# Kernel optimization log

Measured on AMD Instinct MI355X. Metric: run time of the kernel, lower is better.

The kernel has to match this reference:

```python
import jax, jax.numpy as jnp
import numpy as np

B, S, DIM = 2, 2048, 2048
N_HEADS, N_KV = 32, 8
HEAD_DIM = DIM // N_HEADS
N_GROUPS = N_HEADS // N_KV

def setup_inputs() -> dict:
    key = jax.random.key(0)
    kx, kq, kk, kv, ko = jax.random.split(key, 5)
    scale = 1.0 / np.sqrt(DIM)
    return {
        "x": jax.random.normal(kx, (B, S, DIM), dtype=jnp.float32),
        "Wq": jax.random.normal(kq, (DIM, DIM), dtype=jnp.float32) * scale,
        "Wk": jax.random.normal(kk, (DIM, N_KV * HEAD_DIM), dtype=jnp.float32) * scale,
        "Wv": jax.random.normal(kv, (DIM, N_KV * HEAD_DIM), dtype=jnp.float32) * scale,
        "Wo": jax.random.normal(ko, (DIM, DIM), dtype=jnp.float32) * scale,
    }

def reference(x, Wq, Wk, Wv, Wo):
    b, s, _ = x.shape
    sm_scale = HEAD_DIM ** -0.5
    # projections; q grouped as [B, Hk, G, S, D] so kv head i serves q heads i*G..i*G+G-1
    # (matches torch repeat_interleave(n_groups, dim=1))
    q = (x @ Wq).reshape(b, s, N_KV, N_GROUPS, HEAD_DIM)
    k = (x @ Wk).reshape(b, s, N_KV, HEAD_DIM)
    v = (x @ Wv).reshape(b, s, N_KV, HEAD_DIM)
    scores = jnp.einsum("bqhgd,bkhd->bhgqk", q, k) * sm_scale  # [B,Hk,G,S,S]
    attn = jax.nn.softmax(scores, axis=-1)
    out = jnp.einsum("bhgqk,bkhd->bqhgd", attn, v)  # [B,S,Hk,G,D]
    out = out.reshape(b, s, DIM)
    return out @ Wo
```

## Files before the change

kernel.cpp:

```cpp
#include <hip/hip_runtime.h>
#include <hip/hip_bf16.h>

typedef __bf16 bf16x8 __attribute__((ext_vector_type(8)));
typedef float floatx4 __attribute__((ext_vector_type(4)));

#define DIM   2048
#define SEQ   2048
#define BATCH 2
#define NKV   8
#define NGRP  4
#define HDIM  64
#define KVDIM (NKV * HDIM)
#define QKVD  3072

__device__ __forceinline__ ushort f2bf(float f) {
  union { float f; unsigned u; } x; x.f = f;
  return (ushort)((x.u + 0x7fffu + ((x.u >> 16) & 1u)) >> 16);
}
__device__ __forceinline__ unsigned pack_bf2(float a, float b) {
  union { float f; unsigned u; } x, y; x.f = a; y.f = b;
  unsigned ua = x.u + 0x8000u, ub = y.u + 0x8000u;
  return __builtin_amdgcn_perm(ub, ua, 0x07060302);
}
__device__ __forceinline__ unsigned pack_bf2_rn(float a, float b) {
  __hip_bfloat162 h = __float22bfloat162_rn(make_float2(a, b));
  union { __hip_bfloat162 h; unsigned u; } cv; cv.h = h; return cv.u;
}

typedef const __attribute__((address_space(1))) void* gas_t;
typedef __attribute__((address_space(3))) void* las_t;
__device__ __forceinline__ void gload_lds16(const ushort* g, ushort* l) {
  __builtin_amdgcn_global_load_lds((gas_t)g, (las_t)l, 16, 0, 0);
}

__global__ __launch_bounds__(256) void cvt_f2b(
    const float* __restrict__ in, ushort* __restrict__ out)
{
  int i = blockIdx.x * 256 + threadIdx.x;
  const float4* p = (const float4*)in + (size_t)i * 2;
  float4 f0 = p[0], f1 = p[1];
  uint4 v;
  v.x = pack_bf2(f0.x, f0.y); v.y = pack_bf2(f0.z, f0.w);
  v.z = pack_bf2(f1.x, f1.y); v.w = pack_bf2(f1.z, f1.w);
  ((uint4*)out)[i] = v;
}

__global__ __launch_bounds__(256) void transpose_f2b(
    const float* __restrict__ in, ushort* __restrict__ out, int R, int C)
{
  __shared__ ushort tileT[64][72];
  int tr = blockIdx.y * 64;
  int tc = blockIdx.x * 64;
  int row = threadIdx.x >> 2;
  int c16 = (threadIdx.x & 3) * 16;

  ushort arr[16];
  const float* src = in + (size_t)(tr + row) * C + tc + c16;
#pragma unroll
  for (int q = 0; q < 4; ++q) {
    float4 f = *(const float4*)(src + q * 4);
    arr[q * 4 + 0] = f2bf(f.x); arr[q * 4 + 1] = f2bf(f.y);
    arr[q * 4 + 2] = f2bf(f.z); arr[q * 4 + 3] = f2bf(f.w);
  }
  int rot = row & 15;
#pragma unroll
  for (int j = 0; j < 16; ++j) {
    int i2 = (j + rot) & 15;
    tileT[c16 + i2][row] = arr[i2];
  }
  __syncthreads();
  ushort* dst = out + (size_t)(tc + row) * R + tr + c16;
  *(uint4*)dst       = *(const uint4*)&tileT[row][c16];
  *(uint4*)(dst + 8) = *(const uint4*)&tileT[row][c16 + 8];
}

__global__ __launch_bounds__(256) void transpose_b2b(
    const ushort* __restrict__ in, ushort* __restrict__ out,
    int R, int C, int in_stride, size_t in_batch, size_t out_batch)
{
  __shared__ ushort tileT[64][72];
  in  += (size_t)blockIdx.z * in_batch;
  out += (size_t)blockIdx.z * out_batch;
  int tr = blockIdx.y * 64;
  int tc = blockIdx.x * 64;
  int row = threadIdx.x >> 2;
  int c16 = (threadIdx.x & 3) * 16;

  ushort arr[16];
  const ushort* src = in + (size_t)(tr + row) * in_stride + tc + c16;
  *(uint4*)&arr[0] = *(const uint4*)src;
  *(uint4*)&arr[8] = *(const uint4*)(src + 8);
  int rot = row & 15;
#pragma unroll
  for (int j = 0; j < 16; ++j) {
    int i2 = (j + rot) & 15;
    tileT[c16 + i2][row] = arr[i2];
  }
  __syncthreads();
  ushort* dst = out + (size_t)(tc + row) * R + tr + c16;
  *(uint4*)dst       = *(const uint4*)&tileT[row][c16];
  *(uint4*)(dst + 8) = *(const uint4*)&tileT[row][c16 + 8];
}

template<bool CF32>
__global__ __launch_bounds__(256) void gemm_lds(
    const ushort* __restrict__ A, const ushort* __restrict__ Bt,
    void* __restrict__ Cv, int M, int N, int K)
{
  __shared__ ushort As[128 * 32];
  __shared__ ushort Bs[128 * 32];
  int tid  = threadIdx.x;
  int bm   = blockIdx.y * 128;
  int bn   = blockIdx.x * 128;
  int wv   = tid >> 6;
  int ln   = tid & 63;
  int wr   = (wv >> 1) * 64;
  int wc   = (wv & 1) * 64;
  int l15  = ln & 15;
  int quad = ln >> 4;

  int r4 = ln >> 2;
  int c8 = (ln & 3) * 8;
  const ushort* Ag0 = A  + (size_t)(bm + 32 * wv +      r4) * K + c8;
  const ushort* Ag1 = A  + (size_t)(bm + 32 * wv + 16 + r4) * K + c8;
  const ushort* Bg0 = Bt + (size_t)(bn + 32 * wv +      r4) * K + c8;
  const ushort* Bg1 = Bt + (size_t)(bn + 32 * wv + 16 + r4) * K + c8;
  ushort* Al0 = As + 1024 * wv +       ln * 8;
  ushort* Al1 = As + 1024 * wv + 512 + ln * 8;
  ushort* Bl0 = Bs + 1024 * wv +       ln * 8;
  ushort* Bl1 = Bs + 1024 * wv + 512 + ln * 8;

  floatx4 acc[4][4];
#pragma unroll
  for (int i = 0; i < 4; ++i)
#pragma unroll
    for (int j = 0; j < 4; ++j) acc[i][j] = floatx4{0,0,0,0};

  for (int k0 = 0; k0 < K; k0 += 32) {
    __syncthreads();
    gload_lds16(Ag0, Al0);
    gload_lds16(Ag1, Al1);
    gload_lds16(Bg0, Bl0);
    gload_lds16(Bg1, Bl1);
    Ag0 += 32; Ag1 += 32; Bg0 += 32; Bg1 += 32;
    __syncthreads();

    bf16x8 a[4], b[4];
#pragma unroll
    for (int t = 0; t < 4; ++t) {
      a[t] = *(const bf16x8*)&As[(wr + t * 16 + l15) * 32 + quad * 8];
      b[t] = *(const bf16x8*)&Bs[(wc + t * 16 + l15) * 32 + quad * 8];
    }
#pragma unroll
    for (int mt = 0; mt < 4; ++mt)
#pragma unroll
      for (int nt = 0; nt < 4; ++nt)
        acc[mt][nt] = __builtin_amdgcn_mfma_f32_16x16x32_bf16(a[mt], b[nt], acc[mt][nt], 0, 0, 0);
  }

#pragma unroll
  for (int mt = 0; mt < 4; ++mt)
#pragma unroll
    for (int nt = 0; nt < 4; ++nt)
#pragma unroll
      for (int r = 0; r < 4; ++r) {
        size_t idx = (size_t)(bm + wr + mt * 16 + quad * 4 + r) * N
                     + bn + wc + nt * 16 + l15;
        if (CF32) ((float*)Cv)[idx] = acc[mt][nt][r];
        else      ((ushort*)Cv)[idx] = f2bf(acc[mt][nt][r]);
      }
}

#define BM 64
#define BN 64
#define BK 32
#define KP 40

template<bool AF32, bool CF32>
__global__ __launch_bounds__(256) void gemm_abt(
    const void* __restrict__ Av, const ushort* __restrict__ Bt,
    void* __restrict__ Cv, int M, int N, int K)
{
  __shared__ ushort As[BM * KP];
  __shared__ ushort Bs[BN * KP];
  int tid  = threadIdx.x;
  int bm   = blockIdx.y * BM;
  int bn   = blockIdx.x * BN;
  int wave = tid >> 6;
  int lane = tid & 63;
  int wr   = (wave >> 1) * 32;
  int wc   = (wave & 1) * 32;
  int l15  = lane & 15;
  int k8   = (lane >> 4) * 8;

  int srow = tid >> 2;
  int scol = (tid & 3) * 8;

  const float*  Af = (const float*)Av  + (size_t)(bm + srow) * K + scol;
  const ushort* Ah = (const ushort*)Av + (size_t)(bm + srow) * K + scol;
  const ushort* Bp = Bt + (size_t)(bn + srow) * K + scol;

  floatx4 acc00 = {0,0,0,0}, acc01 = {0,0,0,0}, acc10 = {0,0,0,0}, acc11 = {0,0,0,0};

  uint4 av, bv;
  if (AF32) {
    float4 f0 = *(const float4*)Af;
    float4 f1 = *(const float4*)(Af + 4);
    av.x = pack_bf2(f0.x, f0.y); av.y = pack_bf2(f0.z, f0.w);
    av.z = pack_bf2(f1.x, f1.y); av.w = pack_bf2(f1.z, f1.w);
  } else {
    av = *(const uint4*)Ah;
  }
  bv = *(const uint4*)Bp;

  for (int k0 = 0; k0 < K; k0 += BK) {
    __syncthreads();
    *(uint4*)&As[srow * KP + scol] = av;
    *(uint4*)&Bs[srow * KP + scol] = bv;
    __syncthreads();
    if (k0 + BK < K) {
      Af += BK; Ah += BK; Bp += BK;
      if (AF32) {
        float4 f0 = *(const float4*)Af;
        float4 f1 = *(const float4*)(Af + 4);
        av.x = pack_bf2(f0.x, f0.y); av.y = pack_bf2(f0.z, f0.w);
        av.z = pack_bf2(f1.x, f1.y); av.w = pack_bf2(f1.z, f1.w);
      } else {
        av = *(const uint4*)Ah;
      }
      bv = *(const uint4*)Bp;
    }
    bf16x8 a0 = *(const bf16x8*)&As[(wr +      l15) * KP + k8];
    bf16x8 a1 = *(const bf16x8*)&As[(wr + 16 + l15) * KP + k8];
    bf16x8 b0 = *(const bf16x8*)&Bs[(wc +      l15) * KP + k8];
    bf16x8 b1 = *(const bf16x8*)&Bs[(wc + 16 + l15) * KP + k8];
    acc00 = __builtin_amdgcn_mfma_f32_16x16x32_bf16(a0, b0, acc00, 0, 0, 0);
    acc01 = __builtin_amdgcn_mfma_f32_16x16x32_bf16(a0, b1, acc01, 0, 0, 0);
    acc10 = __builtin_amdgcn_mfma_f32_16x16x32_bf16(a1, b0, acc10, 0, 0, 0);
    acc11 = __builtin_amdgcn_mfma_f32_16x16x32_bf16(a1, b1, acc11, 0, 0, 0);
  }

  int rbase = (lane >> 4) * 4;
#pragma unroll
  for (int r = 0; r < 4; ++r) {
    size_t row0 = (size_t)(bm + wr +      rbase + r) * N + bn + wc;
    size_t row1 = (size_t)(bm + wr + 16 + rbase + r) * N + bn + wc;
    if (CF32) {
      float* C = (float*)Cv;
      C[row0 +      l15] = acc00[r];
      C[row0 + 16 + l15] = acc01[r];
      C[row1 +      l15] = acc10[r];
      C[row1 + 16 + l15] = acc11[r];
    } else {
      ushort* C = (ushort*)Cv;
      C[row0 +      l15] = f2bf(acc00[r]);
      C[row0 + 16 + l15] = f2bf(acc01[r]);
      C[row1 +      l15] = f2bf(acc10[r]);
      C[row1 + 16 + l15] = f2bf(acc11[r]);
    }
  }
}

#define GKP 40
template<bool AF32, bool CF32>
__global__ __launch_bounds__(256) void gemm128(
    const void* __restrict__ Av, const ushort* __restrict__ Bt,
    void* __restrict__ Cv, int M, int N, int K)
{
  __shared__ ushort As[128 * GKP];
  __shared__ ushort Bs[128 * GKP];
  int tid  = threadIdx.x;
  int bm   = blockIdx.y * 128;
  int bn   = blockIdx.x * 128;
  int wave = tid >> 6;
  int lane = tid & 63;
  int wr   = (wave >> 1) * 64;
  int wc   = (wave & 1) * 64;
  int l15  = lane & 15;
  int quad = lane >> 4;
  int k8   = quad * 8;

  int srow = tid >> 1;
  int scol = (tid & 1) * 16;

  const float*  Af = (const float*)Av  + (size_t)(bm + srow) * K + scol;
  const ushort* Ah = (const ushort*)Av + (size_t)(bm + srow) * K + scol;
  const ushort* Bp = Bt + (size_t)(bn + srow) * K + scol;

  floatx4 acc[4][4];
#pragma unroll
  for (int i = 0; i < 4; ++i)
#pragma unroll
    for (int j = 0; j < 4; ++j) acc[i][j] = floatx4{0,0,0,0};

  uint4 av0, av1, bv0, bv1;
  if (AF32) {
    float4 f0 = *(const float4*)Af,      f1 = *(const float4*)(Af + 4);
    float4 f2 = *(const float4*)(Af + 8), f3 = *(const float4*)(Af + 12);
    av0.x = pack_bf2(f0.x, f0.y); av0.y = pack_bf2(f0.z, f0.w);
    av0.z = pack_bf2(f1.x, f1.y); av0.w = pack_bf2(f1.z, f1.w);
    av1.x = pack_bf2(f2.x, f2.y); av1.y = pack_bf2(f2.z, f2.w);
    av1.z = pack_bf2(f3.x, f3.y); av1.w = pack_bf2(f3.z, f3.w);
  } else {
    av0 = *(const uint4*)Ah; av1 = *(const uint4*)(Ah + 8);
  }
  bv0 = *(const uint4*)Bp; bv1 = *(const uint4*)(Bp + 8);

  for (int k0 = 0; k0 < K; k0 += 32) {
    __syncthreads();
    *(uint4*)&As[srow * GKP + scol]     = av0;
    *(uint4*)&As[srow * GKP + scol + 8] = av1;
    *(uint4*)&Bs[srow * GKP + scol]     = bv0;
    *(uint4*)&Bs[srow * GKP + scol + 8] = bv1;
    __syncthreads();
    if (k0 + 32 < K) {
      Af += 32; Ah += 32; Bp += 32;
      if (AF32) {
        float4 f0 = *(const float4*)Af,      f1 = *(const float4*)(Af + 4);
        float4 f2 = *(const float4*)(Af + 8), f3 = *(const float4*)(Af + 12);
        av0.x = pack_bf2(f0.x, f0.y); av0.y = pack_bf2(f0.z, f0.w);
        av0.z = pack_bf2(f1.x, f1.y); av0.w = pack_bf2(f1.z, f1.w);
        av1.x = pack_bf2(f2.x, f2.y); av1.y = pack_bf2(f2.z, f2.w);
        av1.z = pack_bf2(f3.x, f3.y); av1.w = pack_bf2(f3.z, f3.w);
      } else {
        av0 = *(const uint4*)Ah; av1 = *(const uint4*)(Ah + 8);
      }
      bv0 = *(const uint4*)Bp; bv1 = *(const uint4*)(Bp + 8);
    }
    bf16x8 a[4], b[4];
#pragma unroll
    for (int t = 0; t < 4; ++t) {
      a[t] = *(const bf16x8*)&As[(wr + t * 16 + l15) * GKP + k8];
      b[t] = *(const bf16x8*)&Bs[(wc + t * 16 + l15) * GKP + k8];
    }
#pragma unroll
    for (int mt = 0; mt < 4; ++mt)
#pragma unroll
      for (int nt = 0; nt < 4; ++nt)
        acc[mt][nt] = __builtin_amdgcn_mfma_f32_16x16x32_bf16(a[mt], b[nt], acc[mt][nt], 0, 0, 0);
  }

#pragma unroll
  for (int mt = 0; mt < 4; ++mt)
#pragma unroll
    for (int nt = 0; nt < 4; ++nt)
#pragma unroll
      for (int r = 0; r < 4; ++r) {
        size_t idx = (size_t)(bm + wr + mt * 16 + quad * 4 + r) * N
                     + bn + wc + nt * 16 + l15;
        if (CF32) ((float*)Cv)[idx] = acc[mt][nt][r];
        else      ((ushort*)Cv)[idx] = f2bf(acc[mt][nt][r]);
      }
}

#define QP 72
#define PP 72

__global__ __launch_bounds__(256) void gqa_attn(
    const ushort* __restrict__ q_buf,
    const ushort* __restrict__ k_buf,
    const ushort* __restrict__ vT,
    ushort* __restrict__ attn)
{
  __shared__ __align__(16) ushort Qs[64 * QP];
  __shared__ __align__(16) ushort Ks[64 * QP];
  __shared__ __align__(16) ushort Vs[64 * QP];
  __shared__ __align__(16) ushort Ps[4][16 * PP];

  int bid = blockIdx.x;
  int qt  = bid & 31;
  int g   = (bid >> 5) & 3;
  int h   = (bid >> 7) & 7;
  int b   = bid >> 10;

  int tid  = threadIdx.x;
  int wave = tid >> 6;
  int lane = tid & 63;
  int l15  = lane & 15;
  int quad = lane >> 4;
  int k8   = quad * 8;

  int srow = tid >> 2;
  int c16  = (tid & 3) * 16;

  {
    const ushort* src = q_buf + (size_t)(b * SEQ + qt * 64 + srow) * DIM
                        + (h * NGRP + g) * HDIM + c16;
    *(uint4*)&Qs[srow * QP + c16]     = *(const uint4*)src;
    *(uint4*)&Qs[srow * QP + c16 + 8] = *(const uint4*)(src + 8);
  }
  __syncthreads();

  bf16x8 bq0 = *(const bf16x8*)&Qs[(wave * 16 + l15) * QP + k8];
  bf16x8 bq1 = *(const bf16x8*)&Qs[(wave * 16 + l15) * QP + 32 + k8];

  float lpart = 0.f;
  floatx4 oarr[4] = {{0,0,0,0},{0,0,0,0},{0,0,0,0},{0,0,0,0}};

  const ushort* kp = k_buf + (size_t)(b * SEQ + srow) * KVDIM + h * HDIM + c16;
  const ushort* vp = vT + ((size_t)(b * NKV + h) * HDIM + srow) * SEQ + c16;

  uint4 kv0 = *(const uint4*)kp;
  uint4 kv1 = *(const uint4*)(kp + 8);
  uint4 vv0 = *(const uint4*)vp;
  uint4 vv1 = *(const uint4*)(vp + 8);

  ushort* Pw = &Ps[wave][0];

  for (int kt = 0; kt < SEQ / 64; ++kt) {
    __syncthreads();
    *(uint4*)&Ks[srow * QP + c16]     = kv0;
    *(uint4*)&Ks[srow * QP + c16 + 8] = kv1;
    *(uint4*)&Vs[srow * QP + c16]     = vv0;
    *(uint4*)&Vs[srow * QP + c16 + 8] = vv1;
    __syncthreads();
    if (kt + 1 < SEQ / 64) {
      kp += (size_t)64 * KVDIM;
      vp += 64;
      kv0 = *(const uint4*)kp;
      kv1 = *(const uint4*)(kp + 8);
      vv0 = *(const uint4*)vp;
      vv1 = *(const uint4*)(vp + 8);
    }

    floatx4 sarr[4];
#pragma unroll
    for (int nt = 0; nt < 4; ++nt) {
      bf16x8 ak0 = *(const bf16x8*)&Ks[(nt * 16 + l15) * QP + k8];
      bf16x8 ak1 = *(const bf16x8*)&Ks[(nt * 16 + l15) * QP + 32 + k8];
      floatx4 s = {0.f, 0.f, 0.f, 0.f};
      s = __builtin_amdgcn_mfma_f32_16x16x32_bf16(ak0, bq0, s, 0, 0, 0);
      s = __builtin_amdgcn_mfma_f32_16x16x32_bf16(ak1, bq1, s, 0, 0, 0);
      sarr[nt] = s;
    }

#pragma unroll
    for (int nt = 0; nt < 4; ++nt) {
      float p0 = __expf(sarr[nt][0] * 0.125f);
      float p1 = __expf(sarr[nt][1] * 0.125f);
      float p2 = __expf(sarr[nt][2] * 0.125f);
      float p3 = __expf(sarr[nt][3] * 0.125f);
      lpart += (p0 + p1) + (p2 + p3);
      uint2 pw;
      pw.x = pack_bf2(p0, p1);
      pw.y = pack_bf2(p2, p3);
      *(uint2*)&Pw[l15 * PP + nt * 16 + quad * 4] = pw;
    }

    bf16x8 ap0 = *(const bf16x8*)&Pw[l15 * PP + k8];
    bf16x8 ap1 = *(const bf16x8*)&Pw[l15 * PP + 32 + k8];
#pragma unroll
    for (int dt = 0; dt < 4; ++dt) {
      bf16x8 bv0q = *(const bf16x8*)&Vs[(dt * 16 + l15) * QP + k8];
      bf16x8 bv1q = *(const bf16x8*)&Vs[(dt * 16 + l15) * QP + 32 + k8];
      oarr[dt] = __builtin_amdgcn_mfma_f32_16x16x32_bf16(ap0, bv0q, oarr[dt], 0, 0, 0);
      oarr[dt] = __builtin_amdgcn_mfma_f32_16x16x32_bf16(ap1, bv1q, oarr[dt], 0, 0, 0);
    }
  }

  float ls = lpart;
  ls += __shfl_xor(ls, 16, 64);
  ls += __shfl_xor(ls, 32, 64);

  __syncthreads();
  float* Lw = (float*)Pw;
  if (quad == 0) Lw[l15] = ls;
  __syncthreads();

#pragma unroll
  for (int r = 0; r < 4; ++r) {
    float inv = 1.0f / Lw[quad * 4 + r];
    int q = qt * 64 + wave * 16 + quad * 4 + r;
    size_t rowoff = (size_t)(b * SEQ + q) * DIM + (h * NGRP + g) * HDIM;
#pragma unroll
    for (int dt = 0; dt < 4; ++dt)
      attn[rowoff + dt * 16 + l15] = f2bf(oarr[dt][r] * inv);
  }
}

__global__ __launch_bounds__(256, 2) void gqa_attn3(
    const ushort* __restrict__ qkv,
    const ushort* __restrict__ vT,
    ushort* __restrict__ attn)
{
  __shared__ __align__(16) ushort Ks[64 * QP];
  __shared__ __align__(16) ushort Vs[64 * QP];
  __shared__ __align__(16) ushort Ps[4][16 * PP];

  int bid = blockIdx.x;
  int qt  = bid & 31;
  int h   = (bid >> 5) & 7;
  int b   = bid >> 8;

  int tid  = threadIdx.x;
  int wave = tid >> 6;
  int lane = tid & 63;
  int l15  = lane & 15;
  int quad = lane >> 4;
  int k8   = quad * 8;

  int srow = tid >> 2;
  int c16  = (tid & 3) * 16;

  bf16x8 bq[NGRP][2];
  {
    const ushort* qrow = qkv + (size_t)(b * SEQ + qt * 64 + wave * 16 + l15) * QKVD
                         + h * NGRP * HDIM;
#pragma unroll
    for (int g = 0; g < NGRP; ++g) {
      bq[g][0] = *(const bf16x8*)(qrow + g * HDIM + k8);
      bq[g][1] = *(const bf16x8*)(qrow + g * HDIM + 32 + k8);
    }
  }
#pragma unroll
  for (int g = 0; g < NGRP; ++g)
#pragma unroll
    for (int j = 0; j < 2; ++j)
#pragma unroll
      for (int e = 0; e < 8; ++e)
        bq[g][j][e] = (__bf16)((float)bq[g][j][e] * 0.125f);

  bf16x8 vones;
#pragma unroll
  for (int i = 0; i < 8; ++i) vones[i] = (__bf16)1.0f;

  floatx4 lacc[NGRP];
  floatx4 oacc[NGRP][4];
#pragma unroll
  for (int g = 0; g < NGRP; ++g) {
    lacc[g] = floatx4{0,0,0,0};
#pragma unroll
    for (int dt = 0; dt < 4; ++dt) oacc[g][dt] = floatx4{0,0,0,0};
  }

  const ushort* kp = qkv + (size_t)(b * SEQ + srow) * QKVD + DIM + h * HDIM + c16;
  const ushort* vp = vT + ((size_t)(b * NKV + h) * HDIM + srow) * SEQ + c16;

  uint4 kv0 = *(const uint4*)kp;
  uint4 kv1 = *(const uint4*)(kp + 8);
  uint4 vv0 = *(const uint4*)vp;
  uint4 vv1 = *(const uint4*)(vp + 8);

  ushort* Pw = &Ps[wave][0];

  for (int kt = 0; kt < SEQ / 64; ++kt) {
    __syncthreads();
    *(uint4*)&Ks[srow * QP + c16]     = kv0;
    *(uint4*)&Ks[srow * QP + c16 + 8] = kv1;
    *(uint4*)&Vs[srow * QP + c16]     = vv0;
    *(uint4*)&Vs[srow * QP + c16 + 8] = vv1;
    __syncthreads();
    if (kt + 1 < SEQ / 64) {
      kp += (size_t)64 * QKVD;
      vp += 64;
      kv0 = *(const uint4*)kp;
      kv1 = *(const uint4*)(kp + 8);
      vv0 = *(const uint4*)vp;
      vv1 = *(const uint4*)(vp + 8);
    }

    bf16x8 ak[4][2], av[4][2];
#pragma unroll
    for (int t = 0; t < 4; ++t) {
      ak[t][0] = *(const bf16x8*)&Ks[(t * 16 + l15) * QP + k8];
      ak[t][1] = *(const bf16x8*)&Ks[(t * 16 + l15) * QP + 32 + k8];
      av[t][0] = *(const bf16x8*)&Vs[(t * 16 + l15) * QP + k8];
      av[t][1] = *(const bf16x8*)&Vs[(t * 16 + l15) * QP + 32 + k8];
    }

#pragma unroll
    for (int g = 0; g < NGRP; ++g) {
#pragma unroll
      for (int nt = 0; nt < 4; ++nt) {
        floatx4 s = {0.f, 0.f, 0.f, 0.f};
        s = __builtin_amdgcn_mfma_f32_16x16x32_bf16(ak[nt][0], bq[g][0], s, 0, 0, 0);
        s = __builtin_amdgcn_mfma_f32_16x16x32_bf16(ak[nt][1], bq[g][1], s, 0, 0, 0);
        float p0 = __expf(s[0]);
        float p1 = __expf(s[1]);
        float p2 = __expf(s[2]);
        float p3 = __expf(s[3]);
        uint2 pw;
        pw.x = pack_bf2_rn(p0, p1);
        pw.y = pack_bf2_rn(p2, p3);
        *(uint2*)&Pw[l15 * PP + nt * 16 + quad * 4] = pw;
      }

      asm volatile("" ::: "memory");

      bf16x8 ap0 = *(const bf16x8*)&Pw[l15 * PP + k8];
      bf16x8 ap1 = *(const bf16x8*)&Pw[l15 * PP + 32 + k8];
      lacc[g] = __builtin_amdgcn_mfma_f32_16x16x32_bf16(ap0, vones, lacc[g], 0, 0, 0);
      lacc[g] = __builtin_amdgcn_mfma_f32_16x16x32_bf16(ap1, vones, lacc[g], 0, 0, 0);
#pragma unroll
      for (int dt = 0; dt < 4; ++dt) {
        oacc[g][dt] = __builtin_amdgcn_mfma_f32_16x16x32_bf16(ap0, av[dt][0], oacc[g][dt], 0, 0, 0);
        oacc[g][dt] = __builtin_amdgcn_mfma_f32_16x16x32_bf16(ap1, av[dt][1], oacc[g][dt], 0, 0, 0);
      }

      asm volatile("" ::: "memory");
    }
  }

#pragma unroll
  for (int g = 0; g < NGRP; ++g) {
#pragma unroll
    for (int r = 0; r < 4; ++r) {
      float inv = 1.0f / lacc[g][r];
      int q = qt * 64 + wave * 16 + quad * 4 + r;
      size_t rowoff = (size_t)(b * SEQ + q) * DIM + (h * NGRP + g) * HDIM;
#pragma unroll
      for (int dt = 0; dt < 4; ++dt)
        attn[rowoff + dt * 16 + l15] = f2bf(oacc[g][dt][r] * inv);
    }
  }
}

extern "C" void kernel_launch(void* const* d_in, const int* in_sizes, int n_in,
                              void* d_out, int out_size, void* d_ws, size_t ws_size,
                              hipStream_t stream)
{
  (void)in_sizes; (void)n_in; (void)out_size;
  const float* x  = (const float*)d_in[0];
  const float* Wq = (const float*)d_in[1];
  const float* Wk = (const float*)d_in[2];
  const float* Wv = (const float*)d_in[3];
  const float* Wo = (const float*)d_in[4];
  float*  outf = (float*)d_out;
  ushort* ob   = (ushort*)d_out;
  ushort* ws16 = (ushort*)d_ws;

  const size_t Mi = 1024 * 1024;
  dim3 blk(256);
  const int M = BATCH * SEQ;

  if (ws_size >= 40u * Mi) {
    ushort* WqkvT = ws16;
    ushort* WoT   = ws16 + 8 * Mi;
    ushort* xb    = ws16 + 12 * Mi;
    ushort* ao    = ws16 + 12 * Mi;
    ushort* qkv   = ob;
    ushort* vt    = ob + 12 * Mi;

    cvt_f2b<<<dim3((M * DIM) / (8 * 256)), blk, 0, stream>>>(x, xb);
    transpose_f2b<<<dim3(DIM / 64,   DIM / 64), blk, 0, stream>>>(Wq, WqkvT, DIM, DIM);
    transpose_f2b<<<dim3(KVDIM / 64, DIM / 64), blk, 0, stream>>>(Wk, WqkvT + 4 * Mi, DIM, KVDIM);
    transpose_f2b<<<dim3(KVDIM / 64, DIM / 64), blk, 0, stream>>>(Wv, WqkvT + 5 * Mi, DIM, KVDIM);
    transpose_f2b<<<dim3(DIM / 64,   DIM / 64), blk, 0, stream>>>(Wo, WoT, DIM, DIM);

    gemm_lds<false><<<dim3(QKVD / 128, M / 128), blk, 0, stream>>>(xb, WqkvT, qkv, M, QKVD, DIM);

    transpose_b2b<<<dim3(KVDIM / 64, SEQ / 64, BATCH), blk, 0, stream>>>(
        qkv + 2560, vt, SEQ, KVDIM, QKVD, (size_t)SEQ * QKVD, (size_t)KVDIM * SEQ);

    gqa_attn3<<<dim3(BATCH * NKV * (SEQ / 64)), blk, 0, stream>>>(qkv, vt, ao);

    gemm_lds<true><<<dim3(DIM / 128, M / 128), blk, 0, stream>>>(ao, WoT, outf, M, DIM, DIM);
  } else {
    ushort* qb  = ob;
    ushort* kb  = ob + 8 * Mi;
    ushort* vb  = ob + 10 * Mi;
    ushort* vt  = ob + 12 * Mi;
    ushort* WqT = ws16;
    ushort* WkT = ws16 + 4 * Mi;
    ushort* WvT = ws16 + 5 * Mi;
    ushort* WoT = ws16 + 8 * Mi;
    ushort* ao  = ws16;

    transpose_f2b<<<dim3(DIM / 64,   DIM / 64), blk, 0, stream>>>(Wq, WqT, DIM, DIM);
    transpose_f2b<<<dim3(KVDIM / 64, DIM / 64), blk, 0, stream>>>(Wk, WkT, DIM, KVDIM);
    transpose_f2b<<<dim3(KVDIM / 64, DIM / 64), blk, 0, stream>>>(Wv, WvT, DIM, KVDIM);
    transpose_f2b<<<dim3(DIM / 64,   DIM / 64), blk, 0, stream>>>(Wo, WoT, DIM, DIM);

    gemm128<true, false><<<dim3(DIM / 128, M / 128), blk, 0, stream>>>(x, WqT, qb, M, DIM, DIM);
    gemm_abt<true, false><<<dim3(KVDIM / BN, M / BM), blk, 0, stream>>>(x, WkT, kb, M, KVDIM, DIM);
    gemm_abt<true, false><<<dim3(KVDIM / BN, M / BM), blk, 0, stream>>>(x, WvT, vb, M, KVDIM, DIM);

    transpose_b2b<<<dim3(KVDIM / 64, SEQ / 64, BATCH), blk, 0, stream>>>(
        vb, vt, SEQ, KVDIM, KVDIM, (size_t)SEQ * KVDIM, (size_t)KVDIM * SEQ);

    gqa_attn<<<dim3(BATCH * NKV * NGRP * (SEQ / 64)), blk, 0, stream>>>(qb, kb, vt, ao);

    gemm128<false, true><<<dim3(DIM / 128, M / 128), blk, 0, stream>>>(ao, WoT, outf, M, DIM, DIM);
  }
}
```

Baseline: 374.0 us.

## Merge weight transposes, widen GEMM K-step, and remap workgroups per XCD

Four separate weight transpose-convert launches are folded into one kernel that picks its source matrix from the block index, which cuts launch overhead. The GEMM now loads two 32-wide K slices per barrier pair, halving the number of synchronisations, at the cost of double the LDS footprint. It also remaps the linear workgroup id so consecutive tiles land on the same XCD, aiming for better L2 reuse. Neither the extra LDS nor the remap adds prefetch overlap, since loads and compute still sit between the same barriers.

```diff
diff --git a/kernel.cpp b/kernel.cpp
--- a/kernel.cpp
+++ b/kernel.cpp
@@ -74,6 +74,46 @@
   *(uint4*)(dst + 8) = *(const uint4*)&tileT[row][c16 + 8];
 }
 
+__global__ __launch_bounds__(256) void transpose_f2b4(
+    const float* __restrict__ Wq, const float* __restrict__ Wk,
+    const float* __restrict__ Wv, const float* __restrict__ Wo,
+    ushort* __restrict__ WqkvT, ushort* __restrict__ WoT)
+{
+  __shared__ ushort tileT[64][72];
+  const size_t Mi = 1024 * 1024;
+  int id = blockIdx.x;
+  const float* in; ushort* out; int C;
+  if (id < 1024)      { in = Wq; out = WqkvT;          C = 2048; }
+  else if (id < 1280) { in = Wk; out = WqkvT + 4 * Mi; C = 512;  id -= 1024; }
+  else if (id < 1536) { in = Wv; out = WqkvT + 5 * Mi; C = 512;  id -= 1280; }
+  else                { in = Wo; out = WoT;            C = 2048; id -= 1536; }
+  const int R = 2048;
+  int nbx = C / 64;
+  int tr = (id / nbx) * 64;
+  int tc = (id % nbx) * 64;
+  int row = threadIdx.x >> 2;
+  int c16 = (threadIdx.x & 3) * 16;
+
+  ushort arr[16];
+  const float* src = in + (size_t)(tr + row) * C + tc + c16;
+#pragma unroll
+  for (int q = 0; q < 4; ++q) {
+    float4 f = *(const float4*)(src + q * 4);
+    arr[q * 4 + 0] = f2bf(f.x); arr[q * 4 + 1] = f2bf(f.y);
+    arr[q * 4 + 2] = f2bf(f.z); arr[q * 4 + 3] = f2bf(f.w);
+  }
+  int rot = row & 15;
+#pragma unroll
+  for (int j = 0; j < 16; ++j) {
+    int i2 = (j + rot) & 15;
+    tileT[c16 + i2][row] = arr[i2];
+  }
+  __syncthreads();
+  ushort* dst = out + (size_t)(tc + row) * R + tr + c16;
+  *(uint4*)dst       = *(const uint4*)&tileT[row][c16];
+  *(uint4*)(dst + 8) = *(const uint4*)&tileT[row][c16 + 8];
+}
+
 __global__ __launch_bounds__(256) void transpose_b2b(
     const ushort* __restrict__ in, ushort* __restrict__ out,
     int R, int C, int in_stride, size_t in_batch, size_t out_batch)
@@ -107,11 +147,20 @@
     const ushort* __restrict__ A, const ushort* __restrict__ Bt,
     void* __restrict__ Cv, int M, int N, int K)
 {
-  __shared__ ushort As[128 * 32];
-  __shared__ ushort Bs[128 * 32];
+  __shared__ ushort As[2][128 * 32];
+  __shared__ ushort Bs[2][128 * 32];
   int tid  = threadIdx.x;
-  int bm   = blockIdx.y * 128;
-  int bn   = blockIdx.x * 128;
+
+  int gx  = gridDim.x;
+  int nwg = gx * gridDim.y;
+  int lin = blockIdx.y * gx + blockIdx.x;
+  if ((nwg & 7) == 0) {
+    int cpx = nwg >> 3;
+    lin = (lin & 7) * cpx + (lin >> 3);
+  }
+  int bm = (lin / gx) * 128;
+  int bn = (lin % gx) * 128;
+
   int wv   = tid >> 6;
   int ln   = tid & 63;
   int wr   = (wv >> 1) * 64;
@@ -121,14 +170,19 @@
 
   int r4 = ln >> 2;
   int c8 = (ln & 3) * 8;
-  const ushort* Ag0 = A  + (size_t)(bm + 32 * wv +      r4) * K + c8;
-  const ushort* Ag1 = A  + (size_t)(bm + 32 * wv + 16 + r4) * K + c8;
-  const ushort* Bg0 = Bt + (size_t)(bn + 32 * wv +      r4) * K + c8;
-  const ushort* Bg1 = Bt + (size_t)(bn + 32 * wv + 16 + r4) * K + c8;
-  ushort* Al0 = As + 1024 * wv +       ln * 8;
-  ushort* Al1 = As + 1024 * wv + 512 + ln * 8;
-  ushort* Bl0 = Bs + 1024 * wv +       ln * 8;
-  ushort* Bl1 = Bs + 1024 * wv + 512 + ln * 8;
+  const ushort* Ag[2][2];
+  const ushort* Bg[2][2];
+  ushort* Al[2][2];
+  ushort* Bl[2][2];
+#pragma unroll
+  for (int h = 0; h < 2; ++h)
+#pragma unroll
+    for (int i = 0; i < 2; ++i) {
+      Ag[h][i] = A  + (size_t)(bm + 32 * wv + 16 * i + r4) * K + 32 * h + c8;
+      Bg[h][i] = Bt + (size_t)(bn + 32 * wv + 16 * i + r4) * K + 32 * h + c8;
+      Al[h][i] = &As[h][0] + 1024 * wv + 512 * i + ln * 8;
+      Bl[h][i] = &Bs[h][0] + 1024 * wv + 512 * i + ln * 8;
+    }
 
   floatx4 acc[4][4];
 #pragma unroll
@@ -136,26 +190,32 @@
 #pragma unroll
     for (int j = 0; j < 4; ++j) acc[i][j] = floatx4{0,0,0,0};
 
-  for (int k0 = 0; k0 < K; k0 += 32) {
-    __syncthreads();
-    gload_lds16(Ag0, Al0);
-    gload_lds16(Ag1, Al1);
-    gload_lds16(Bg0, Bl0);
-    gload_lds16(Bg1, Bl1);
-    Ag0 += 32; Ag1 += 32; Bg0 += 32; Bg1 += 32;
-    __syncthreads();
-
-    bf16x8 a[4], b[4];
-#pragma unroll
-    for (int t = 0; t < 4; ++t) {
-      a[t] = *(const bf16x8*)&As[(wr + t * 16 + l15) * 32 + quad * 8];
-      b[t] = *(const bf16x8*)&Bs[(wc + t * 16 + l15) * 32 + quad * 8];
-    }
-#pragma unroll
-    for (int mt = 0; mt < 4; ++mt)
-#pragma unroll
-      for (int nt = 0; nt < 4; ++nt)
-        acc[mt][nt] = __builtin_amdgcn_mfma_f32_16x16x32_bf16(a[mt], b[nt], acc[mt][nt], 0, 0, 0);
+  for (int k0 = 0; k0 < K; k0 += 64) {
+    __syncthreads();
+#pragma unroll
+    for (int h = 0; h < 2; ++h)
+#pragma unroll
+      for (int i = 0; i < 2; ++i) {
+        gload_lds16(Ag[h][i], Al[h][i]);
+        gload_lds16(Bg[h][i], Bl[h][i]);
+        Ag[h][i] += 64; Bg[h][i] += 64;
+      }
+    __syncthreads();
+
+#pragma unroll
+    for (int h = 0; h < 2; ++h) {
+      bf16x8 a[4], b[4];
+#pragma unroll
+      for (int t = 0; t < 4; ++t) {
+        a[t] = *(const bf16x8*)&As[h][(wr + t * 16 + l15) * 32 + quad * 8];
+        b[t] = *(const bf16x8*)&Bs[h][(wc + t * 16 + l15) * 32 + quad * 8];
+      }
+#pragma unroll
+      for (int mt = 0; mt < 4; ++mt)
+#pragma unroll
+        for (int nt = 0; nt < 4; ++nt)
+          acc[mt][nt] = __builtin_amdgcn_mfma_f32_16x16x32_bf16(a[mt], b[nt], acc[mt][nt], 0, 0, 0);
+    }
   }
 
 #pragma unroll
@@ -642,10 +702,7 @@
     ushort* vt    = ob + 12 * Mi;
 
     cvt_f2b<<<dim3((M * DIM) / (8 * 256)), blk, 0, stream>>>(x, xb);
-    transpose_f2b<<<dim3(DIM / 64,   DIM / 64), blk, 0, stream>>>(Wq, WqkvT, DIM, DIM);
-    transpose_f2b<<<dim3(KVDIM / 64, DIM / 64), blk, 0, stream>>>(Wk, WqkvT + 4 * Mi, DIM, KVDIM);
-    transpose_f2b<<<dim3(KVDIM / 64, DIM / 64), blk, 0, stream>>>(Wv, WqkvT + 5 * Mi, DIM, KVDIM);
-    transpose_f2b<<<dim3(DIM / 64,   DIM / 64), blk, 0, stream>>>(Wo, WoT, DIM, DIM);
+    transpose_f2b4<<<dim3(2560), blk, 0, stream>>>(Wq, Wk, Wv, Wo, WqkvT, WoT);
 
     gemm_lds<false><<<dim3(QKVD / 128, M / 128), blk, 0, stream>>>(xb, WqkvT, qkv, M, QKVD, DIM);
 
```

Measured after the change: 347.1 us. 7.2% less time.
